# Kernel optimization log

Hardware: AMD Instinct MI355X
Metric: run time of the kernel (lower is better)

The kernel has to match this reference:

```python
import jax, jax.numpy as jnp
import numpy as np

SIGMA_MAX = 0.3
GAMMA = 1.0
COV_SHRINK = 0.1
COV_DELTA = 1e-3
BN_EPS = 1e-5
PATCH = 3


def setup_inputs() -> dict:
    key = jax.random.key(0)
    ks = jax.random.split(key, 5)
    B, K, C, H, W = 2, 8, 64, 128, 128
    X = jax.random.normal(ks[0], (B, K, C, H, W), dtype=jnp.float32)
    w1 = jax.random.normal(ks[1], (C // 2, C), dtype=jnp.float32) * 0.1
    w2 = jax.random.normal(ks[2], (1, C // 2), dtype=jnp.float32) * 0.1
    return {
        "X": X,
        "w1": w1,
        "bn_scale": jnp.ones((C // 2,), jnp.float32),
        "bn_bias": jnp.zeros((C // 2,), jnp.float32),
        "bn_mean": jnp.zeros((C // 2,), jnp.float32),
        "bn_var": jnp.ones((C // 2,), jnp.float32),
        "w2": w2,
        "a0_raw": jax.random.normal(ks[3], (K,), dtype=jnp.float32) * 0.1,
        "sigma_raw": jax.random.normal(ks[4], (K,), dtype=jnp.float32) * 0.1,
    }


def _forward(X, w1, bn_scale, bn_bias, bn_mean, bn_var, w2, a0_raw, sigma_raw):
    B, K, C, H, W = X.shape
    # --- SensorMapGenerator: 1x1 conv -> BN (inference) -> ReLU -> 1x1 conv ---
    Xf = X.reshape(B * K, C, H, W)
    h = jnp.einsum('oc,bchw->bohw', w1, Xf)                       # [BK, C/2, H, W]
    inv_std = bn_scale / jnp.sqrt(bn_var + BN_EPS)
    h = h * inv_std[None, :, None, None] + (bn_bias - bn_mean * inv_std)[None, :, None, None]
    h = jax.nn.relu(h)
    S = jnp.einsum('oc,bchw->bohw', w2, h).reshape(B, K, H, W)    # scalar sensor maps

    # --- CovarianceEstimator: reflect pad, 3x3 patches, center, R = PP^T/N ---
    pad = PATCH // 2
    Sp = jnp.pad(S, ((0, 0), (0, 0), (pad, pad), (pad, pad)), mode='reflect')
    patches = jnp.stack(
        [Sp[:, :, i:i + H, j:j + W] for i in range(PATCH) for j in range(PATCH)],
        axis=-1)                                                  # [B, K, H, W, N]
    N = PATCH * PATCH
    patches = patches.transpose(0, 2, 3, 1, 4)                    # [B, H, W, K, N]
    pc = patches - patches.mean(axis=-1, keepdims=True)
    R = jnp.matmul(pc, pc.swapaxes(-1, -2)) / N                   # [B, H, W, K, K]

    # --- Guidance vector and uncertainty (stage mode) ---
    a0 = jax.nn.softmax(a0_raw)                                   # [K], sums to 1
    sigma = SIGMA_MAX * jax.nn.sigmoid(sigma_raw)                 # [K]

    # --- Robust diagonal-loaded Capon solve per pixel ---
    # R_reg = (1-shrink)*R + shrink*(tr R / K)*I + delta*I + gamma*diag(sigma^2)
    I = jnp.eye(K, dtype=R.dtype)
    tr = jnp.trace(R, axis1=-2, axis2=-1)                         # [B, H, W]
    load = COV_DELTA * I + GAMMA * jnp.diag(sigma * sigma)
    R_load = (1.0 - COV_SHRINK) * R + (COV_SHRINK * tr / K)[..., None, None] * I + load
    rhs = jnp.broadcast_to(a0[:, None], R_load.shape[:-2] + (K, 1))
    w_un = jnp.linalg.solve(R_load, rhs)[..., 0]                  # [B, H, W, K]
    denom = jnp.einsum('bhwk,k->bhw', w_un, a0)
    w = w_un / denom[..., None]                                   # a0^T w = 1

    # --- Weighted fusion over streams ---
    Y = jnp.einsum('bhwk,bkchw->bchw', w, X)                      # [B, C, H, W]
    return Y


def reference(X, w1, bn_scale, bn_bias, bn_mean, bn_var, w2, a0_raw, sigma_raw):
    return _forward(X, w1, bn_scale, bn_bias, bn_mean, bn_var, w2, a0_raw, sigma_raw)
```

## Files before the change

### kernel.cpp

```cpp
#include <hip/hip_runtime.h>
#include <hip/hip_bf16.h>
#include <math.h>

#define B_    2
#define K_    8
#define C_    64
#define CH_   32
#define H_    128
#define W_    128
#define HW_   16384
#define BN_EPS 1e-5f
#define SIGMA_MAX 0.3f
#define COV_SHRINK 0.1f
#define COV_DELTA 1e-3f

__global__ void __launch_bounds__(256)
stage1_kernel(const float* __restrict__ X,
              const float* __restrict__ w1,
              const float* __restrict__ bn_scale,
              const float* __restrict__ bn_bias,
              const float* __restrict__ bn_mean,
              const float* __restrict__ bn_var,
              const float* __restrict__ w2,
              float* __restrict__ S) {
    int idx = blockIdx.x * blockDim.x + threadIdx.x;
    int hw = idx & (HW_ - 1);
    int bk = idx >> 14;
    const float* xp = X + (size_t)bk * (C_ * HW_) + hw;

    float x[C_];
#pragma unroll
    for (int c = 0; c < C_; ++c) x[c] = xp[(size_t)c * HW_];

    float out = 0.f;
#pragma unroll
    for (int o = 0; o < CH_; ++o) {
        const float* wrow = w1 + o * C_;
        float s0 = 0.f, s1 = 0.f, s2 = 0.f, s3 = 0.f;
#pragma unroll
        for (int c = 0; c < C_; c += 4) {
            s0 = fmaf(wrow[c],     x[c],     s0);
            s1 = fmaf(wrow[c + 1], x[c + 1], s1);
            s2 = fmaf(wrow[c + 2], x[c + 2], s2);
            s3 = fmaf(wrow[c + 3], x[c + 3], s3);
        }
        float s = (s0 + s1) + (s2 + s3);
        float inv = bn_scale[o] * rsqrtf(bn_var[o] + BN_EPS);
        float h = fmaf(s, inv, fmaf(-bn_mean[o], inv, bn_bias[o]));
        out = fmaf(w2[o], fmaxf(h, 0.f), out);
    }
    S[idx] = out;
}

__global__ void capon_kernel(const float* __restrict__ S,
                             const float* __restrict__ a0_raw,
                             const float* __restrict__ sigma_raw,
                             float* __restrict__ wOut) {
    int idx = blockIdx.x * blockDim.x + threadIdx.x;
    int b  = idx >> 14;
    int hw = idx & (HW_ - 1);
    int h  = hw >> 7;
    int w  = hw & (W_ - 1);

    float a0[K_], sig2[K_];
    {
        float m = -1e30f;
#pragma unroll
        for (int i = 0; i < K_; ++i) m = fmaxf(m, a0_raw[i]);
        float sum = 0.f;
#pragma unroll
        for (int i = 0; i < K_; ++i) { a0[i] = __expf(a0_raw[i] - m); sum += a0[i]; }
        float invs = 1.f / sum;
#pragma unroll
        for (int i = 0; i < K_; ++i) a0[i] *= invs;
#pragma unroll
        for (int i = 0; i < K_; ++i) {
            float sg = SIGMA_MAX / (1.f + __expf(-sigma_raw[i]));
            sig2[i] = sg * sg;
        }
    }

    int hm = (h == 0)      ? 1       : h - 1;
    int hp = (h == H_ - 1) ? H_ - 2  : h + 1;
    int wm = (w == 0)      ? 1       : w - 1;
    int wp = (w == W_ - 1) ? W_ - 2  : w + 1;
    int rows[3] = {hm * W_, h * W_, hp * W_};
    int cols[3] = {wm, w, wp};

    float pc[K_][9];
#pragma unroll
    for (int k = 0; k < K_; ++k) {
        const float* sp = S + (((size_t)b * K_ + k) << 14);
        float p[9];
        float m = 0.f;
#pragma unroll
        for (int i = 0; i < 3; ++i)
#pragma unroll
            for (int j = 0; j < 3; ++j) {
                float v = sp[rows[i] + cols[j]];
                p[i * 3 + j] = v;
                m += v;
            }
        m *= (1.f / 9.f);
#pragma unroll
        for (int n = 0; n < 9; ++n) pc[k][n] = p[n] - m;
    }

    float A[K_][K_];
    float tr = 0.f;
#pragma unroll
    for (int i = 0; i < K_; ++i) {
        float s = 0.f;
#pragma unroll
        for (int n = 0; n < 9; ++n) s = fmaf(pc[i][n], pc[i][n], s);
        s *= (1.f / 9.f);
        tr += s;
        A[i][i] = s;
    }
#pragma unroll
    for (int i = 0; i < K_; ++i)
#pragma unroll
        for (int j = 0; j < i; ++j) {
            float s = 0.f;
#pragma unroll
            for (int n = 0; n < 9; ++n) s = fmaf(pc[i][n], pc[j][n], s);
            A[i][j] = (1.f - COV_SHRINK) * s * (1.f / 9.f);
        }
    float dl = COV_SHRINK * tr * (1.f / (float)K_) + COV_DELTA;
#pragma unroll
    for (int i = 0; i < K_; ++i)
        A[i][i] = (1.f - COV_SHRINK) * A[i][i] + dl + sig2[i];

#pragma unroll
    for (int j = 0; j < K_; ++j) {
        float d = A[j][j];
#pragma unroll
        for (int t = 0; t < j; ++t) d = fmaf(-A[j][t], A[j][t], d);
        d = sqrtf(d);
        A[j][j] = d;
        float inv = 1.f / d;
#pragma unroll
        for (int i = j + 1; i < K_; ++i) {
            float s = A[i][j];
#pragma unroll
            for (int t = 0; t < j; ++t) s = fmaf(-A[i][t], A[j][t], s);
            A[i][j] = s * inv;
        }
    }
    float z[K_];
#pragma unroll
    for (int i = 0; i < K_; ++i) {
        float s = a0[i];
#pragma unroll
        for (int t = 0; t < i; ++t) s = fmaf(-A[i][t], z[t], s);
        z[i] = s / A[i][i];
    }
    float x[K_];
#pragma unroll
    for (int i = K_ - 1; i >= 0; --i) {
        float s = z[i];
#pragma unroll
        for (int t = i + 1; t < K_; ++t) s = fmaf(-A[t][i], x[t], s);
        x[i] = s / A[i][i];
    }
    float denom = 0.f;
#pragma unroll
    for (int k = 0; k < K_; ++k) denom = fmaf(x[k], a0[k], denom);
    float invd = 1.f / denom;

    float4 o0 = make_float4(x[0] * invd, x[1] * invd, x[2] * invd, x[3] * invd);
    float4 o1 = make_float4(x[4] * invd, x[5] * invd, x[6] * invd, x[7] * invd);
    float4* dst = (float4*)(wOut + (size_t)idx * K_);
    dst[0] = o0;
    dst[1] = o1;
}

__global__ void __launch_bounds__(256)
fuse_kernel(const float* __restrict__ X,
            const float* __restrict__ wW,
            float* __restrict__ out) {
    int idx = blockIdx.x * blockDim.x + threadIdx.x;
    int hw = idx & (HW_ - 1);
    int bc = idx >> 14;
    int b = bc >> 6;
    int c = bc & (C_ - 1);
    size_t pix = ((size_t)b << 14) + hw;

    const float4* wv4 = (const float4*)(wW + pix * K_);
    float4 wa = wv4[0];
    float4 wb = wv4[1];

    const float* xp = X + (((size_t)b * K_) * C_ + c) * HW_ + hw;
    const size_t kstride = (size_t)C_ * HW_;

    float acc;
    acc = wa.x * xp[0];
    acc = fmaf(wa.y, xp[kstride * 1], acc);
    acc = fmaf(wa.z, xp[kstride * 2], acc);
    acc = fmaf(wa.w, xp[kstride * 3], acc);
    acc = fmaf(wb.x, xp[kstride * 4], acc);
    acc = fmaf(wb.y, xp[kstride * 5], acc);
    acc = fmaf(wb.z, xp[kstride * 6], acc);
    acc = fmaf(wb.w, xp[kstride * 7], acc);
    __builtin_nontemporal_store(acc, &out[idx]);
}

extern "C" void kernel_launch(void* const* d_in, const int* in_sizes, int n_in,
                              void* d_out, int out_size, void* d_ws, size_t ws_size,
                              hipStream_t stream) {
    const float* X         = (const float*)d_in[0];
    const float* w1        = (const float*)d_in[1];
    const float* bn_scale  = (const float*)d_in[2];
    const float* bn_bias   = (const float*)d_in[3];
    const float* bn_mean   = (const float*)d_in[4];
    const float* bn_var    = (const float*)d_in[5];
    const float* w2        = (const float*)d_in[6];
    const float* a0_raw    = (const float*)d_in[7];
    const float* sigma_raw = (const float*)d_in[8];
    float* out = (float*)d_out;
    float* ws  = (float*)d_ws;

    float* S  = ws;
    float* wW = ws + (B_ * K_ * HW_);

    int n1 = B_ * K_ * HW_;
    stage1_kernel<<<n1 / 256, 256, 0, stream>>>(X, w1, bn_scale, bn_bias,
                                                bn_mean, bn_var, w2, S);

    int n2 = B_ * HW_;
    capon_kernel<<<n2 / 256, 256, 0, stream>>>(S, a0_raw, sigma_raw, wW);

    int n3 = B_ * C_ * HW_;
    fuse_kernel<<<n3 / 256, 256, 0, stream>>>(X, wW, out);
}
```

Baseline: 159.3 us.

## Fold BN into weights via prep kernel and compute two pixels per thread

Adds a small prep kernel that folds the batch-norm scale into a transposed w1 and precomputes the effective bias, so stage1 no longer recomputes rsqrt per output channel. Stage1 now processes two adjacent pixels per thread with float2 loads and 32-wide accumulators per pixel, reusing each weight across both pixels. The loop is reordered to stream channels instead of holding all 64 inputs in registers. The Capon launch block size also drops to 64 threads. The cost is an extra launch and higher register pressure from 64 accumulators, bounded by launch_bounds(256,4).

```diff
diff --git a/kernel.cpp b/kernel.cpp
--- a/kernel.cpp
+++ b/kernel.cpp
@@ -14,42 +14,59 @@
 #define COV_SHRINK 0.1f
 #define COV_DELTA 1e-3f
 
-__global__ void __launch_bounds__(256)
+__global__ void prep_kernel(const float* __restrict__ w1,
+                            const float* __restrict__ bn_scale,
+                            const float* __restrict__ bn_bias,
+                            const float* __restrict__ bn_mean,
+                            const float* __restrict__ bn_var,
+                            const float* __restrict__ w2,
+                            float* __restrict__ par) {
+    int t = threadIdx.x;
+    for (int i = t; i < CH_ * C_; i += blockDim.x) {
+        int c = i >> 5;
+        int o = i & 31;
+        float inv = bn_scale[o] * rsqrtf(bn_var[o] + BN_EPS);
+        par[c * CH_ + o] = w1[o * C_ + c] * inv;
+    }
+    if (t < CH_) {
+        float inv = bn_scale[t] * rsqrtf(bn_var[t] + BN_EPS);
+        par[2048 + t] = bn_bias[t] - bn_mean[t] * inv;
+        par[2080 + t] = w2[t];
+    }
+}
+
+__global__ void __launch_bounds__(256, 4)
 stage1_kernel(const float* __restrict__ X,
-              const float* __restrict__ w1,
-              const float* __restrict__ bn_scale,
-              const float* __restrict__ bn_bias,
-              const float* __restrict__ bn_mean,
-              const float* __restrict__ bn_var,
-              const float* __restrict__ w2,
+              const float* __restrict__ wf,
+              const float* __restrict__ beff,
+              const float* __restrict__ w2c,
               float* __restrict__ S) {
-    int idx = blockIdx.x * blockDim.x + threadIdx.x;
-    int hw = idx & (HW_ - 1);
-    int bk = idx >> 14;
-    const float* xp = X + (size_t)bk * (C_ * HW_) + hw;
-
-    float x[C_];
-#pragma unroll
-    for (int c = 0; c < C_; ++c) x[c] = xp[(size_t)c * HW_];
-
-    float out = 0.f;
+    int t = blockIdx.x * blockDim.x + threadIdx.x;
+    int hw2 = t & (HW_ / 2 - 1);
+    int bk  = t >> 13;
+    const float2* xp = (const float2*)(X + (size_t)bk * (C_ * HW_)) + hw2;
+
+    float acc0[CH_], acc1[CH_];
+#pragma unroll
+    for (int o = 0; o < CH_; ++o) { acc0[o] = beff[o]; acc1[o] = beff[o]; }
+
+#pragma unroll 8
+    for (int c = 0; c < C_; ++c) {
+        float2 xv = xp[(size_t)c * (HW_ / 2)];
+        const float* wrow = wf + c * CH_;
+#pragma unroll
+        for (int o = 0; o < CH_; ++o) {
+            acc0[o] = fmaf(wrow[o], xv.x, acc0[o]);
+            acc1[o] = fmaf(wrow[o], xv.y, acc1[o]);
+        }
+    }
+    float s0 = 0.f, s1 = 0.f;
 #pragma unroll
     for (int o = 0; o < CH_; ++o) {
-        const float* wrow = w1 + o * C_;
-        float s0 = 0.f, s1 = 0.f, s2 = 0.f, s3 = 0.f;
-#pragma unroll
-        for (int c = 0; c < C_; c += 4) {
-            s0 = fmaf(wrow[c],     x[c],     s0);
-            s1 = fmaf(wrow[c + 1], x[c + 1], s1);
-            s2 = fmaf(wrow[c + 2], x[c + 2], s2);
-            s3 = fmaf(wrow[c + 3], x[c + 3], s3);
-        }
-        float s = (s0 + s1) + (s2 + s3);
-        float inv = bn_scale[o] * rsqrtf(bn_var[o] + BN_EPS);
-        float h = fmaf(s, inv, fmaf(-bn_mean[o], inv, bn_bias[o]));
-        out = fmaf(w2[o], fmaxf(h, 0.f), out);
-    }
-    S[idx] = out;
+        s0 = fmaf(w2c[o], fmaxf(acc0[o], 0.f), s0);
+        s1 = fmaf(w2c[o], fmaxf(acc1[o], 0.f), s1);
+    }
+    ((float2*)S)[t] = make_float2(s0, s1);
 }
 
 __global__ void capon_kernel(const float* __restrict__ S,
@@ -220,15 +237,18 @@
     float* out = (float*)d_out;
     float* ws  = (float*)d_ws;
 
-    float* S  = ws;
-    float* wW = ws + (B_ * K_ * HW_);
-
-    int n1 = B_ * K_ * HW_;
-    stage1_kernel<<<n1 / 256, 256, 0, stream>>>(X, w1, bn_scale, bn_bias,
-                                                bn_mean, bn_var, w2, S);
+    float* par = ws;
+    float* S   = ws + 4096;
+    float* wW  = ws + 4096 + (B_ * K_ * HW_);
+
+    prep_kernel<<<1, 256, 0, stream>>>(w1, bn_scale, bn_bias, bn_mean, bn_var,
+                                       w2, par);
+
+    int n1 = B_ * K_ * HW_ / 2;
+    stage1_kernel<<<n1 / 256, 256, 0, stream>>>(X, par, par + 2048, par + 2080, S);
 
     int n2 = B_ * HW_;
-    capon_kernel<<<n2 / 256, 256, 0, stream>>>(S, a0_raw, sigma_raw, wW);
+    capon_kernel<<<n2 / 64, 64, 0, stream>>>(S, a0_raw, sigma_raw, wW);
 
     int n3 = B_ * C_ * HW_;
     fuse_kernel<<<n3 / 256, 256, 0, stream>>>(X, wW, out);
```

Measured after the change: 156.4 us. No clear change (-1.8%).
